# Kernel tuning notes

Measured on AMD Instinct MI355X. Metric: run time of the kernel, lower is better.

## Reference

```python
import jax, jax.numpy as jnp
import numpy as np

D_MODEL = 1024
N_HEADS = 16
D_HEAD = 64
TOTAL = N_HEADS * D_HEAD


def setup_inputs() -> dict:
    key = jax.random.key(0)
    k1, k2, k3 = jax.random.split(key, 3)
    x = jax.random.normal(k1, (2, 2048, D_MODEL), dtype=jnp.float32)
    W_qkv = jax.random.normal(k2, (3 * TOTAL, D_MODEL), dtype=jnp.float32) * 0.02
    W_out = jax.random.normal(k3, (D_MODEL, TOTAL), dtype=jnp.float32) * 0.02
    return {"x": x, "W_qkv": W_qkv, "W_out": W_out}


def reference(x, W_qkv, W_out):
    B, T, D = x.shape
    scale = D_HEAD ** -0.5
    qkv = jnp.einsum('btd,ed->bte', x, W_qkv)  # [B,T,3*TOTAL]
    q, k, v = jnp.split(qkv, 3, axis=-1)
    def heads(t):
        return t.reshape(B, T, N_HEADS, D_HEAD).transpose(0, 2, 1, 3)  # [B,H,T,Dh]
    q, k, v = heads(q), heads(k), heads(v)
    scores = jnp.einsum('bhqd,bhkd->bhqk', q, k) * scale
    causal = jnp.tril(jnp.ones((T, T), dtype=bool))
    scores = jnp.where(causal[None, None], scores, -jnp.inf)
    attn = jax.nn.softmax(scores, axis=-1)
    out = jnp.einsum('bhqk,bhkd->bhqd', attn, v)
    out = out.transpose(0, 2, 1, 3).reshape(B, T, TOTAL)
    return jnp.einsum('bte,de->btd', out, W_out)
```

## Files before the change

kernel.cpp:

```cpp
#include <hip/hip_runtime.h>
#include <hip/hip_bf16.h>

typedef __attribute__((ext_vector_type(4))) float f32x4;
typedef __attribute__((ext_vector_type(8))) short s16x8;
typedef __attribute__((ext_vector_type(4))) short s16x4;

#define DEV static __device__ __forceinline__

DEV unsigned short f2bf(float f) {
    unsigned int u = __builtin_bit_cast(unsigned int, f);
    u += 0x7fffu + ((u >> 16) & 1u);
    return (unsigned short)(u >> 16);
}

#if __has_builtin(__builtin_amdgcn_exp2f)
#define EXP2(x) __builtin_amdgcn_exp2f(x)
#else
#define EXP2(x) exp2f(x)
#endif

DEV unsigned int pack2(float a, float b) {
#if __has_builtin(__builtin_amdgcn_perm)
    return __builtin_amdgcn_perm(__builtin_bit_cast(unsigned int, b),
                                 __builtin_bit_cast(unsigned int, a), 0x07060302u);
#else
    return (__builtin_bit_cast(unsigned int, a) >> 16) |
           (__builtin_bit_cast(unsigned int, b) & 0xffff0000u);
#endif
}

DEV s16x8 ld8(const unsigned short* p) {
    s16x4 lo = *(const s16x4*)(p);
    s16x4 hi = *(const s16x4*)(p + 4);
    return __builtin_shufflevector(lo, hi, 0, 1, 2, 3, 4, 5, 6, 7);
}
DEV s16x8 ld8a(const unsigned short* p) { return *(const s16x8*)p; }

DEV f32x4 mfma16(s16x8 a, s16x8 b, f32x4 c) {
    return __builtin_amdgcn_mfma_f32_16x16x32_bf16(a, b, c, 0, 0, 0);
}

DEV void glds16(const unsigned short* g, unsigned short* l) {
    __builtin_amdgcn_global_load_lds(
        (const __attribute__((address_space(1))) unsigned int*)g,
        (__attribute__((address_space(3))) unsigned int*)l, 16, 0, 0);
}

__global__ __launch_bounds__(256) void convf2b2(
        const float* __restrict__ s0, unsigned short* __restrict__ d0, int n40,
        const float* __restrict__ s1, unsigned short* __restrict__ d1, int n41) {
    int i = blockIdx.x * 256 + threadIdx.x;
    if (i < n40) {
        float4 v = ((const float4*)s0)[i];
        s16x4 o = {(short)f2bf(v.x), (short)f2bf(v.y), (short)f2bf(v.z), (short)f2bf(v.w)};
        ((s16x4*)d0)[i] = o;
    } else if (i - n40 < n41) {
        int j = i - n40;
        float4 v = ((const float4*)s1)[j];
        s16x4 o = {(short)f2bf(v.x), (short)f2bf(v.y), (short)f2bf(v.z), (short)f2bf(v.w)};
        ((s16x4*)d1)[j] = o;
    }
}

__global__ __launch_bounds__(256) void convf2b(const float* __restrict__ s,
                                               unsigned short* __restrict__ d, int n4) {
    int i = blockIdx.x * 256 + threadIdx.x;
    if (i < n4) {
        float4 v = ((const float4*)s)[i];
        s16x4 o = {(short)f2bf(v.x), (short)f2bf(v.y), (short)f2bf(v.z), (short)f2bf(v.w)};
        ((s16x4*)d)[i] = o;
    }
}

__global__ __launch_bounds__(512) void qkv_gemm(
        const unsigned short* __restrict__ Xb, const unsigned short* __restrict__ Wq,
        unsigned short* __restrict__ q_ws, unsigned short* __restrict__ k_ws,
        unsigned short* __restrict__ v_ws) {
    __shared__ unsigned short As[2][128 * 32];
    __shared__ unsigned short Bs[2][128 * 32];
    const int tid = threadIdx.x, lane = tid & 63, wave = tid >> 6;
    const int l15 = lane & 15, l4 = lane >> 4;
    const int wm = (wave >> 1) * 32, wn = (wave & 1) * 64;
    const int m0 = blockIdx.y * 128, n0 = blockIdx.x * 128;

    f32x4 acc[2][4];
    for (int i = 0; i < 2; i++)
        for (int j = 0; j < 4; j++) acc[i][j] = (f32x4){0.f, 0.f, 0.f, 0.f};

    const unsigned short* aptr = &Xb[(size_t)(m0 + wave * 16 + (lane >> 2)) * 1024 + (lane & 3) * 8];
    const unsigned short* bptr = &Wq[(size_t)(n0 + wave * 16 + (lane >> 2)) * 1024 + (lane & 3) * 8];

    for (int k0 = 0; k0 < 1024; k0 += 64) {
        __syncthreads();
        for (int c = 0; c < 2; c++) {
            glds16(aptr + k0 + c * 32, &As[c][(wave * 16) * 32]);
            glds16(bptr + k0 + c * 32, &Bs[c][(wave * 16) * 32]);
        }
        __syncthreads();
        for (int c = 0; c < 2; c++) {
            s16x8 af[2], bf[4];
            for (int mt = 0; mt < 2; mt++) af[mt] = ld8a(&As[c][(wm + mt * 16 + l15) * 32 + l4 * 8]);
            for (int nt = 0; nt < 4; nt++) bf[nt] = ld8a(&Bs[c][(wn + nt * 16 + l15) * 32 + l4 * 8]);
            for (int mt = 0; mt < 2; mt++)
                for (int nt = 0; nt < 4; nt++)
                    acc[mt][nt] = mfma16(af[mt], bf[nt], acc[mt][nt]);
        }
    }

    const int gnb = n0 + wn;
    const int which = gnb >> 10, h = (gnb >> 6) & 15;
    const int bidx = m0 >> 11, tb = m0 & 2047;
    if (which == 2) {
        unsigned short* dst = v_ws + (size_t)(bidx * 16 + h) * 64 * 2048;
        for (int mt = 0; mt < 2; mt++) {
            int t = tb + wm + mt * 16 + l4 * 4;
            for (int nt = 0; nt < 4; nt++) {
                int dh = nt * 16 + l15;
                s16x4 pp;
                for (int r = 0; r < 4; r++) pp[r] = (short)f2bf(acc[mt][nt][r]);
                *(s16x4*)&dst[(size_t)dh * 2048 + t] = pp;
            }
        }
    } else {
        unsigned short* dst = ((which == 0) ? q_ws : k_ws) + (size_t)(bidx * 16 + h) * 2048 * 64;
        const float sc = (which == 0) ? 0.18033688f : 1.0f;
        for (int mt = 0; mt < 2; mt++) {
            int t0 = tb + wm + mt * 16 + l4 * 4;
            for (int nt = 0; nt < 4; nt++) {
                int dh = nt * 16 + l15;
                for (int r = 0; r < 4; r++)
                    dst[(size_t)(t0 + r) * 64 + dh] = f2bf(acc[mt][nt][r] * sc);
            }
        }
    }
}

__global__ __launch_bounds__(256) void attn(
        const unsigned short* __restrict__ q_ws, const unsigned short* __restrict__ k_ws,
        const unsigned short* __restrict__ v_ws, unsigned short* __restrict__ ao) {
    constexpr int LDP = 68;
    __shared__ unsigned short Ks[2][2][64 * 32];
    __shared__ unsigned short Vt[2][2][64 * 32];
    __shared__ unsigned short Ps[4 * 32 * LDP];
    const int tid = threadIdx.x, lane = tid & 63, wave = tid >> 6;
    const int l15 = lane & 15, l4 = lane >> 4;
    const int bh = blockIdx.x, b = bh >> 4, h = bh & 15;
    const int yy = blockIdx.y;
    const int qtile = (yy < 8) ? (15 - yy) : (yy - 8);
    const int q0 = qtile * 128;
    const int qw0 = q0 + wave * 32;
    const size_t base = (size_t)bh * 2048 * 64;
    const unsigned short* vtb = v_ws + (size_t)bh * 64 * 2048;
    unsigned short* Pw = &Ps[wave * 32 * LDP];

    const int seg = wave;
    const unsigned short* kg0[2];
    const unsigned short* vg0[2];
    unsigned short* kl[2][2];
    unsigned short* vl[2][2];
    for (int hf = 0; hf < 2; hf++) {
        kg0[hf] = &k_ws[base + (size_t)(seg * 16 + (lane >> 2)) * 64 + hf * 32 + (lane & 3) * 8];
        vg0[hf] = &vtb[(size_t)(seg * 16 + (lane >> 2)) * 2048 + hf * 32 + (lane & 3) * 8];
        for (int bu = 0; bu < 2; bu++) {
            kl[bu][hf] = &Ks[bu][hf][(seg * 16) * 32];
            vl[bu][hf] = &Vt[bu][hf][(seg * 16) * 32];
        }
    }

    s16x8 qf[2][2];
    for (int qs = 0; qs < 2; qs++)
        for (int c = 0; c < 2; c++)
            qf[qs][c] = ld8a(&q_ws[base + (size_t)(qw0 + qs * 16 + l15) * 64 + c * 32 + l4 * 8]);

    f32x4 o[2][4];
    for (int qs = 0; qs < 2; qs++)
        for (int i = 0; i < 4; i++) o[qs][i] = (f32x4){0.f, 0.f, 0.f, 0.f};
    float lsum[2] = {0.f, 0.f};

    for (int hf = 0; hf < 2; hf++) {
        glds16(kg0[hf], kl[0][hf]);
        glds16(vg0[hf], vl[0][hf]);
    }

    const int kend = q0 + 128;
    for (int k0 = 0; k0 < kend; k0 += 64) {
        const int cur = (k0 >> 6) & 1;
        __syncthreads();
        if (k0 + 64 < kend) {
            for (int hf = 0; hf < 2; hf++) {
                glds16(kg0[hf] + (size_t)(k0 + 64) * 64, kl[cur ^ 1][hf]);
                glds16(vg0[hf] + (k0 + 64), vl[cur ^ 1][hf]);
            }
        }

        if (k0 < qw0 + 32) {
            f32x4 st[2][4];
            for (int qs = 0; qs < 2; qs++)
                for (int ks = 0; ks < 4; ks++) st[qs][ks] = (f32x4){0.f, 0.f, 0.f, 0.f};
            for (int c = 0; c < 2; c++)
                for (int ks = 0; ks < 4; ks++) {
                    s16x8 kf = ld8a(&Ks[cur][c][(ks * 16 + l15) * 32 + l4 * 8]);
                    st[0][ks] = mfma16(kf, qf[0][c], st[0][ks]);
                    st[1][ks] = mfma16(kf, qf[1][c], st[1][ks]);
                }

            if (k0 + 63 > qw0) {
                for (int qs = 0; qs < 2; qs++) {
                    int qg = qw0 + qs * 16 + l15;
                    for (int ks = 0; ks < 4; ks++)
                        for (int r = 0; r < 4; r++) {
                            int kg = k0 + ks * 16 + l4 * 4 + r;
                            if (kg > qg) st[qs][ks][r] = -1e30f;
                        }
                }
            }
            for (int qs = 0; qs < 2; qs++) {
                float part = 0.f;
                for (int ks = 0; ks < 4; ks++) {
                    float p0 = EXP2(st[qs][ks][0]);
                    float p1 = EXP2(st[qs][ks][1]);
                    float p2 = EXP2(st[qs][ks][2]);
                    float p3 = EXP2(st[qs][ks][3]);
                    part += (p0 + p1) + (p2 + p3);
                    unsigned int u0 = pack2(p0, p1), u1 = pack2(p2, p3);
                    *(uint2*)&Pw[(qs * 16 + l15) * LDP + ks * 16 + l4 * 4] = (uint2){u0, u1};
                }
                lsum[qs] += part;
            }

            s16x8 pf[2][2];
            for (int qs = 0; qs < 2; qs++)
                for (int c = 0; c < 2; c++)
                    pf[qs][c] = ld8(&Pw[(qs * 16 + l15) * LDP + c * 32 + l4 * 8]);
            for (int c = 0; c < 2; c++)
                for (int ds = 0; ds < 4; ds++) {
                    s16x8 vf = ld8a(&Vt[cur][c][(ds * 16 + l15) * 32 + l4 * 8]);
                    o[0][ds] = mfma16(vf, pf[0][c], o[0][ds]);
                    o[1][ds] = mfma16(vf, pf[1][c], o[1][ds]);
                }
        }
    }

    for (int qs = 0; qs < 2; qs++) {
        float t = lsum[qs];
        t += __shfl_xor(t, 16, 64);
        t += __shfl_xor(t, 32, 64);
        float inv = 1.f / t;
        for (int ds = 0; ds < 4; ds++) {
            s16x4 pp;
            for (int r = 0; r < 4; r++) pp[r] = (short)f2bf(o[qs][ds][r] * inv);
            *(s16x4*)&Pw[(qs * 16 + l15) * LDP + ds * 16 + l4 * 4] = pp;
        }
    }
    for (int qs = 0; qs < 2; qs++) {
        int qr = lane >> 2, qc = lane & 3;
        size_t orow = ((size_t)b * 2048 + q0 + wave * 32 + qs * 16 + qr) * 1024 + h * 64 + qc * 16;
        *(s16x8*)&ao[orow]     = ld8(&Pw[(qs * 16 + qr) * LDP + qc * 16]);
        *(s16x8*)&ao[orow + 8] = ld8(&Pw[(qs * 16 + qr) * LDP + qc * 16 + 8]);
    }
}

__global__ __launch_bounds__(256) void out_gemm(
        const unsigned short* __restrict__ A, const unsigned short* __restrict__ Bm,
        float* __restrict__ OUT) {
    __shared__ unsigned short As[2][128 * 32];
    __shared__ unsigned short Bs[2][64 * 32];
    const int tid = threadIdx.x, lane = tid & 63, wave = tid >> 6;
    const int l15 = lane & 15, l4 = lane >> 4;
    const int wm = wave * 32;
    const int m0 = blockIdx.y * 128, n0 = blockIdx.x * 64;

    f32x4 acc[2][4];
    for (int i = 0; i < 2; i++)
        for (int j = 0; j < 4; j++) acc[i][j] = (f32x4){0.f, 0.f, 0.f, 0.f};

    const unsigned short* aptr = &A[(size_t)(m0 + wave * 32 + (lane >> 2)) * 1024 + (lane & 3) * 8];
    const unsigned short* bptr = &Bm[(size_t)(n0 + wave * 16 + (lane >> 2)) * 1024 + (lane & 3) * 8];

    for (int k0 = 0; k0 < 1024; k0 += 64) {
        __syncthreads();
        for (int c = 0; c < 2; c++) {
            glds16(aptr + k0 + c * 32, &As[c][(wave * 32) * 32]);
            glds16(aptr + k0 + c * 32 + 16 * 1024, &As[c][(wave * 32 + 16) * 32]);
            glds16(bptr + k0 + c * 32, &Bs[c][(wave * 16) * 32]);
        }
        __syncthreads();
        for (int c = 0; c < 2; c++) {
            s16x8 af[2], bf[4];
            for (int mt = 0; mt < 2; mt++) af[mt] = ld8a(&As[c][(wm + mt * 16 + l15) * 32 + l4 * 8]);
            for (int nt = 0; nt < 4; nt++) bf[nt] = ld8a(&Bs[c][(nt * 16 + l15) * 32 + l4 * 8]);
            for (int mt = 0; mt < 2; mt++)
                for (int nt = 0; nt < 4; nt++)
                    acc[mt][nt] = mfma16(af[mt], bf[nt], acc[mt][nt]);
        }
    }

    for (int mt = 0; mt < 2; mt++)
        for (int nt = 0; nt < 4; nt++)
            for (int r = 0; r < 4; r++) {
                int gm = m0 + wm + mt * 16 + l4 * 4 + r;
                int gn = n0 + nt * 16 + l15;
                OUT[(size_t)gm * 1024 + gn] = acc[mt][nt][r];
            }
}

extern "C" void kernel_launch(void* const* d_in, const int* in_sizes, int n_in,
                              void* d_out, int out_size, void* d_ws, size_t ws_size,
                              hipStream_t stream) {
    (void)in_sizes; (void)n_in; (void)out_size; (void)ws_size;
    const float* x    = (const float*)d_in[0];
    const float* Wqkv = (const float*)d_in[1];
    const float* Wout = (const float*)d_in[2];
    float* out = (float*)d_out;

    unsigned short* q_ws = (unsigned short*)d_ws;
    unsigned short* k_ws = q_ws + (size_t)4 * 1024 * 1024;
    unsigned short* v_ws = k_ws + (size_t)4 * 1024 * 1024;
    unsigned short* xb   = v_ws + (size_t)4 * 1024 * 1024;
    unsigned short* ao   = xb;
    unsigned short* wqb  = (unsigned short*)d_out;
    unsigned short* wob  = q_ws;

    const int n4x = 2 * 2048 * 1024 / 4, n4w = 3072 * 1024 / 4;
    convf2b2<<<(n4x + n4w + 255) / 256, 256, 0, stream>>>(x, xb, n4x, Wqkv, wqb, n4w);
    qkv_gemm<<<dim3(24, 32), 512, 0, stream>>>(xb, wqb, q_ws, k_ws, v_ws);
    attn<<<dim3(32, 16), 256, 0, stream>>>(q_ws, k_ws, v_ws, ao);
    convf2b<<<1024, 256, 0, stream>>>(Wout, wob, 1024 * 1024 / 4);
    out_gemm<<<dim3(16, 32), 256, 0, stream>>>(ao, wob, out);
}
```

Before: 177.5 us.

## Balance causal attention by pairing mirrored query tiles and swizzling LDS

```diff
diff --git a/kernel.cpp b/kernel.cpp
--- a/kernel.cpp
+++ b/kernel.cpp
@@ -45,6 +45,9 @@
         (const __attribute__((address_space(1))) unsigned int*)g,
         (__attribute__((address_space(3))) unsigned int*)l, 16, 0, 0);
 }
+
+struct QS1 { static constexpr int v = 1; };
+struct QS2 { static constexpr int v = 2; };
 
 __global__ __launch_bounds__(256) void convf2b2(
         const float* __restrict__ s0, unsigned short* __restrict__ d0, int n40,
@@ -144,23 +147,31 @@
     __shared__ unsigned short Ps[4 * 32 * LDP];
     const int tid = threadIdx.x, lane = tid & 63, wave = tid >> 6;
     const int l15 = lane & 15, l4 = lane >> 4;
-    const int bh = blockIdx.x, b = bh >> 4, h = bh & 15;
-    const int yy = blockIdx.y;
-    const int qtile = (yy < 8) ? (15 - yy) : (yy - 8);
-    const int q0 = qtile * 128;
-    const int qw0 = q0 + wave * 32;
+    const int xf = (l15 >> 1) & 3;
+
+    const int id = blockIdx.x;
+    const int bh8 = id & 7, rest = id >> 3;
+    const int qq = rest & 15, g = rest >> 4;
+    const int bh = bh8 + 8 * g, b = bh >> 4, h = bh & 15;
+    const int p = (g < 2) ? qq : 15 - qq;
+    const int rb[2] = {(31 - p) * 64 + wave * 16,
+                       p * 64 + wave * 16};
+    const int kend = (32 - p) * 64;
+
     const size_t base = (size_t)bh * 2048 * 64;
     const unsigned short* vtb = v_ws + (size_t)bh * 64 * 2048;
     unsigned short* Pw = &Ps[wave * 32 * LDP];
 
     const int seg = wave;
+    const int srow = lane >> 2;
+    const int scol = ((lane & 3) ^ ((lane >> 3) & 3)) * 8;
     const unsigned short* kg0[2];
     const unsigned short* vg0[2];
     unsigned short* kl[2][2];
     unsigned short* vl[2][2];
     for (int hf = 0; hf < 2; hf++) {
-        kg0[hf] = &k_ws[base + (size_t)(seg * 16 + (lane >> 2)) * 64 + hf * 32 + (lane & 3) * 8];
-        vg0[hf] = &vtb[(size_t)(seg * 16 + (lane >> 2)) * 2048 + hf * 32 + (lane & 3) * 8];
+        kg0[hf] = &k_ws[base + (size_t)(seg * 16 + srow) * 64 + hf * 32 + scol];
+        vg0[hf] = &vtb[(size_t)(seg * 16 + srow) * 2048 + hf * 32 + scol];
         for (int bu = 0; bu < 2; bu++) {
             kl[bu][hf] = &Ks[bu][hf][(seg * 16) * 32];
             vl[bu][hf] = &Vt[bu][hf][(seg * 16) * 32];
@@ -170,7 +181,7 @@
     s16x8 qf[2][2];
     for (int qs = 0; qs < 2; qs++)
         for (int c = 0; c < 2; c++)
-            qf[qs][c] = ld8a(&q_ws[base + (size_t)(qw0 + qs * 16 + l15) * 64 + c * 32 + l4 * 8]);
+            qf[qs][c] = ld8a(&q_ws[base + (size_t)(rb[qs] + l15) * 64 + c * 32 + l4 * 8]);
 
     f32x4 o[2][4];
     for (int qs = 0; qs < 2; qs++)
@@ -182,7 +193,6 @@
         glds16(vg0[hf], vl[0][hf]);
     }
 
-    const int kend = q0 + 128;
     for (int k0 = 0; k0 < kend; k0 += 64) {
         const int cur = (k0 >> 6) & 1;
         __syncthreads();
@@ -193,28 +203,30 @@
             }
         }
 
-        if (k0 < qw0 + 32) {
-            f32x4 st[2][4];
-            for (int qs = 0; qs < 2; qs++)
+        auto tile = [&](auto tag) {
+            constexpr int NQS = decltype(tag)::v;
+            f32x4 st[NQS][4];
+            for (int qs = 0; qs < NQS; qs++)
                 for (int ks = 0; ks < 4; ks++) st[qs][ks] = (f32x4){0.f, 0.f, 0.f, 0.f};
+            __builtin_amdgcn_s_setprio(1);
             for (int c = 0; c < 2; c++)
                 for (int ks = 0; ks < 4; ks++) {
-                    s16x8 kf = ld8a(&Ks[cur][c][(ks * 16 + l15) * 32 + l4 * 8]);
-                    st[0][ks] = mfma16(kf, qf[0][c], st[0][ks]);
-                    st[1][ks] = mfma16(kf, qf[1][c], st[1][ks]);
+                    s16x8 kf = ld8a(&Ks[cur][c][(ks * 16 + l15) * 32 + (l4 ^ xf) * 8]);
+                    for (int qs = 0; qs < NQS; qs++)
+                        st[qs][ks] = mfma16(kf, qf[qs][c], st[qs][ks]);
                 }
-
-            if (k0 + 63 > qw0) {
-                for (int qs = 0; qs < 2; qs++) {
-                    int qg = qw0 + qs * 16 + l15;
+            __builtin_amdgcn_s_setprio(0);
+
+            for (int qs = 0; qs < NQS; qs++)
+                if (k0 + 63 > rb[qs]) {
+                    int qg = rb[qs] + l15;
                     for (int ks = 0; ks < 4; ks++)
                         for (int r = 0; r < 4; r++) {
                             int kg = k0 + ks * 16 + l4 * 4 + r;
                             if (kg > qg) st[qs][ks][r] = -1e30f;
                         }
                 }
-            }
-            for (int qs = 0; qs < 2; qs++) {
+            for (int qs = 0; qs < NQS; qs++) {
                 float part = 0.f;
                 for (int ks = 0; ks < 4; ks++) {
                     float p0 = EXP2(st[qs][ks][0]);
@@ -228,17 +240,22 @@
                 lsum[qs] += part;
             }
 
-            s16x8 pf[2][2];
-            for (int qs = 0; qs < 2; qs++)
+            s16x8 pf[NQS][2];
+            for (int qs = 0; qs < NQS; qs++)
                 for (int c = 0; c < 2; c++)
                     pf[qs][c] = ld8(&Pw[(qs * 16 + l15) * LDP + c * 32 + l4 * 8]);
+            __builtin_amdgcn_s_setprio(1);
             for (int c = 0; c < 2; c++)
                 for (int ds = 0; ds < 4; ds++) {
-                    s16x8 vf = ld8a(&Vt[cur][c][(ds * 16 + l15) * 32 + l4 * 8]);
-                    o[0][ds] = mfma16(vf, pf[0][c], o[0][ds]);
-                    o[1][ds] = mfma16(vf, pf[1][c], o[1][ds]);
+                    s16x8 vf = ld8a(&Vt[cur][c][(ds * 16 + l15) * 32 + (l4 ^ xf) * 8]);
+                    for (int qs = 0; qs < NQS; qs++)
+                        o[qs][ds] = mfma16(vf, pf[qs][c], o[qs][ds]);
                 }
-        }
+            __builtin_amdgcn_s_setprio(0);
+        };
+
+        if (k0 < rb[1] + 16) tile(QS2{});
+        else                 tile(QS1{});
     }
 
     for (int qs = 0; qs < 2; qs++) {
@@ -254,7 +271,7 @@
     }
     for (int qs = 0; qs < 2; qs++) {
         int qr = lane >> 2, qc = lane & 3;
-        size_t orow = ((size_t)b * 2048 + q0 + wave * 32 + qs * 16 + qr) * 1024 + h * 64 + qc * 16;
+        size_t orow = ((size_t)b * 2048 + rb[qs] + qr) * 1024 + h * 64 + qc * 16;
         *(s16x8*)&ao[orow]     = ld8(&Pw[(qs * 16 + qr) * LDP + qc * 16]);
         *(s16x8*)&ao[orow + 8] = ld8(&Pw[(qs * 16 + qr) * LDP + qc * 16 + 8]);
     }
@@ -324,7 +341,7 @@
     const int n4x = 2 * 2048 * 1024 / 4, n4w = 3072 * 1024 / 4;
     convf2b2<<<(n4x + n4w + 255) / 256, 256, 0, stream>>>(x, xb, n4x, Wqkv, wqb, n4w);
     qkv_gemm<<<dim3(24, 32), 512, 0, stream>>>(xb, wqb, q_ws, k_ws, v_ws);
-    attn<<<dim3(32, 16), 256, 0, stream>>>(q_ws, k_ws, v_ws, ao);
+    attn<<<dim3(512), 256, 0, stream>>>(q_ws, k_ws, v_ws, ao);
     convf2b<<<1024, 256, 0, stream>>>(Wout, wob, 1024 * 1024 / 4);
     out_gemm<<<dim3(16, 32), 256, 0, stream>>>(ao, wob, out);
 }
```

After: 170.9 us. 1.04x faster.
